# Performance work log

Measured on AMD Instinct MI355X. Metric: run time of the kernel, lower is better.

Reference implementation:

```python
import jax, jax.numpy as jnp
import numpy as np

BIG = 1e30  # stands in for sys.maxsize in fp32-safe form


def _find_neg_anchors(e_actv, host):
    # Full pairwise Euclidean distance matrix (equivalent to the
    # pdist -> triangular reconstruction in the torch code).
    sq = jnp.sum(e_actv * e_actv, axis=1)                       # [n]
    d2 = sq[:, None] + sq[None, :] - 2.0 * (e_actv @ e_actv.T)  # [n, n]
    dist = jnp.sqrt(jnp.maximum(d2, 0.0))
    n = e_actv.shape[0]
    # mask: self (diagonal) and same-discriminator pairs -> huge distance
    same_discr = host[:, None] == host[None, :]
    eye = jnp.eye(n, dtype=bool)
    dist = jnp.where(same_discr | eye, BIG, dist)
    idxs = jnp.argmin(dist, axis=1)                             # [n]
    return e_actv[idxs]                                         # gather


def setup_inputs() -> dict:
    key = jax.random.key(0)
    k1, k2, k3 = jax.random.split(key, 3)
    n, d = 8192, 256
    e_actv = jax.random.normal(k1, (n, d), dtype=jnp.float32)
    e_ap = jax.random.normal(k2, (n, d), dtype=jnp.float32)
    host = jax.random.randint(k3, (n,), 0, 64, dtype=jnp.int64 if jax.config.read('jax_enable_x64') else jnp.int32)
    return {"e_actv": e_actv, "e_ap": e_ap, "host": host}


def reference(e_actv, e_ap, host):
    # forward returns (e_actv, e_ap, e_an); e_an computed under no_grad
    e_an = jax.lax.stop_gradient(_find_neg_anchors(e_actv, host))
    return (e_actv, e_ap, e_an)
```

## Files before the change

### kernel.cpp

```cpp
#include <hip/hip_runtime.h>
#include <hip/hip_bf16.h>
#include <cmath>
#include <cstddef>

#define N 8192
#define D 256
#define BIR 128
#define BJC 64
#define NBLK 4160

typedef __attribute__((ext_vector_type(8))) short short8;
typedef __attribute__((ext_vector_type(4))) float float4v;

__device__ inline ushort f2bf(float x) {
    __hip_bfloat16 h = __float2bfloat16(x);
    return __builtin_bit_cast(ushort, h);
}
__device__ inline float bf2f(ushort u) {
    __hip_bfloat16 h = __builtin_bit_cast(__hip_bfloat16, u);
    return __bfloat162float(h);
}

__device__ inline unsigned long long packKI(float k, int idx) {
    unsigned u = __float_as_uint(k);
    u = (u & 0x80000000u) ? ~u : (u | 0x80000000u);
    return ((unsigned long long)u << 32) | (unsigned)idx;
}


__global__ void prep_kernel(const float4* __restrict__ a, const float4* __restrict__ p,
                            float4* __restrict__ out, float* __restrict__ sq,
                            ushort* __restrict__ Ehi, ushort* __restrict__ Elo,
                            unsigned long long* __restrict__ M) {
    const int gsz = gridDim.x * blockDim.x;
    const int g0 = blockIdx.x * blockDim.x + threadIdx.x;
    const int total = N * D / 4;

    for (int idx = g0; idx < total; idx += gsz) {
        float4 v = a[idx];
        out[idx] = v;
        float s = v.x * v.x + v.y * v.y + v.z * v.z + v.w * v.w;
        #pragma unroll
        for (int off = 32; off; off >>= 1) s += __shfl_down(s, off);
        if ((threadIdx.x & 63) == 0) sq[idx >> 6] = s;
    }
    for (int idx = g0; idx < total; idx += gsz) out[total + idx] = p[idx];

    {
        const int w = g0 >> 6;
        if (w < 4096) {
            const int lane = threadIdx.x & 63;
            const int tx = lane & 15;
            const int q  = lane >> 4;
            const int r16 = w >> 3;
            const int ktc = w & 7;
            const int row = r16 * 16 + tx;
            const float4 v0 = a[row * 64 + ktc * 8 + q * 2];
            const float4 v1 = a[row * 64 + ktc * 8 + q * 2 + 1];
            float e[8] = {v0.x, v0.y, v0.z, v0.w, v1.x, v1.y, v1.z, v1.w};
            short8 hs, ls;
            #pragma unroll
            for (int j = 0; j < 8; j++) {
                ushort h = f2bf(e[j]);
                ushort l = f2bf(e[j] - bf2f(h));
                hs[j] = (short)h;
                ls[j] = (short)l;
            }
            const size_t off = (size_t)(r16 * 8 + ktc) * 512 + lane * 8;
            *(short8*)&Ehi[off] = hs;
            *(short8*)&Elo[off] = ls;
        }
    }
    for (int i = g0; i < N; i += gsz) M[i] = 0xFFFFFFFFFFFFFFFFull;
}

__launch_bounds__(256, 4)
__global__ void argmin_sym(const ushort* __restrict__ Ehi, const ushort* __restrict__ Elo,
                           const int* __restrict__ host, const float* __restrict__ sq,
                           unsigned long long* __restrict__ M) {
    const int b0 = blockIdx.x;
    const int b = (b0 & 7) * (NBLK / 8) + (b0 >> 3);

    int g, p;
    if (b < 1808)      { g = 0; p = b; }
    else if (b < 3104) { g = 1; p = b - 1808; }
    else if (b < 3888) { g = 2; p = b - 3104; }
    else               { g = 3; p = b - 3888; }
    int d, i;
    if (p >= 240) {
        d = 30 + ((p - 240) >> 4);
        i = (p - 240) & 15;
    } else {
        int m = (int)sqrtf((float)p);
        while (m * m > p) m--;
        while ((m + 1) * (m + 1) <= p) m++;
        if (p >= m * m + m) { d = 2 * m;     i = p - (m * m + m); }
        else                { d = 2 * m - 1; i = p - m * m; }
    }
    const int ti = 16 * g + i;
    const int tj = 32 * g + d;

    __shared__ float sqA_s[BIR];
    __shared__ float sqB_s[BJC];
    __shared__ int   hostB_s[BJC];
    __shared__ float rowV[2 * BIR]; __shared__ int rowI[2 * BIR];
    __shared__ float colV[2 * BJC]; __shared__ int colI[2 * BJC];

    const int ib0 = ti * BIR;
    const int jb0 = tj * BJC;
    const int tid = threadIdx.x;
    const int lane = tid & 63;
    const int wave = tid >> 6;
    const int wrow = wave >> 1;
    const int wcol = wave & 1;
    const int tx = lane & 15;
    const int q  = lane >> 4;

    if (tid < BIR) sqA_s[tid] = sq[ib0 + tid];
    if (tid < BJC) {
        sqB_s[tid] = sq[jb0 + tid];
        hostB_s[tid] = host[jb0 + tid];
    }

    unsigned hostAp[4];
    #pragma unroll
    for (int rt = 0; rt < 4; rt++) {
        unsigned pk = 0;
        #pragma unroll
        for (int reg = 0; reg < 4; reg++) {
            int hv = host[ib0 + wrow * 64 + rt * 16 + q * 4 + reg];
            pk |= ((unsigned)hv & 0xFFu) << (8 * reg);
        }
        hostAp[rt] = pk;
    }

    float4v acc[4][2];
    #pragma unroll
    for (int rt = 0; rt < 4; rt++)
        #pragma unroll
        for (int ct = 0; ct < 2; ct++) acc[rt][ct] = (float4v)(0.0f);

    const int pA = (ib0 >> 4) + wrow * 4;
    const int pB = (jb0 >> 4) + wcol * 2;
    const int lo8 = lane * 8;

    int obA[4], obB[2];
    #pragma unroll
    for (int rt = 0; rt < 4; rt++) obA[rt] = (((pA + rt) * 8) * 512 + lo8) * 2;
    #pragma unroll
    for (int ct = 0; ct < 2; ct++) obB[ct] = (((pB + ct) * 8) * 512 + lo8) * 2;
    const char* EhiB = (const char*)Ehi;
    const char* EloB = (const char*)Elo;

    short8 aH[4], aL[4], bH[2], bL[2];

    #pragma unroll
    for (int k = 0; k < 8; k++) {
        #pragma unroll
        for (int rt = 0; rt < 4; rt++) {
            aH[rt] = *(const short8*)(EhiB + obA[rt]);
            aL[rt] = *(const short8*)(EloB + obA[rt]);
        }
        #pragma unroll
        for (int ct = 0; ct < 2; ct++) {
            bH[ct] = *(const short8*)(EhiB + obB[ct]);
            bL[ct] = *(const short8*)(EloB + obB[ct]);
        }
        #pragma unroll
        for (int rt = 0; rt < 4; rt++) obA[rt] += 1024;
        #pragma unroll
        for (int ct = 0; ct < 2; ct++) obB[ct] += 1024;
        __builtin_amdgcn_sched_barrier(0);
        #pragma unroll
        for (int rt = 0; rt < 4; rt++)
            #pragma unroll
            for (int ct = 0; ct < 2; ct++)
                acc[rt][ct] = __builtin_amdgcn_mfma_f32_16x16x32_bf16(aH[rt], bH[ct], acc[rt][ct], 0, 0, 0);
        #pragma unroll
        for (int rt = 0; rt < 4; rt++)
            #pragma unroll
            for (int ct = 0; ct < 2; ct++)
                acc[rt][ct] = __builtin_amdgcn_mfma_f32_16x16x32_bf16(aH[rt], bL[ct], acc[rt][ct], 0, 0, 0);
        #pragma unroll
        for (int rt = 0; rt < 4; rt++)
            #pragma unroll
            for (int ct = 0; ct < 2; ct++)
                acc[rt][ct] = __builtin_amdgcn_mfma_f32_16x16x32_bf16(aL[rt], bH[ct], acc[rt][ct], 0, 0, 0);
        __builtin_amdgcn_sched_barrier(0);
    }

    __syncthreads();

    #pragma unroll
    for (int rt = 0; rt < 4; rt++) {
        unsigned hp = hostAp[rt];
        #pragma unroll
        for (int reg = 0; reg < 4; reg++) {
            int il = wrow * 64 + rt * 16 + q * 4 + reg;
            int ig = ib0 + il;
            int ha = (int)((hp >> (8 * reg)) & 0xFFu);
            float v = 3.0e38f; int ix = 0x7fffffff;
            #pragma unroll
            for (int ct = 0; ct < 2; ct++) {
                int jl = wcol * 32 + ct * 16 + tx;
                int jg = jb0 + jl;
                float key = sqB_s[jl] - 2.0f * acc[rt][ct][reg];
                bool masked = (hostB_s[jl] == ha) || (jg <= ig);
                if (!masked && (key < v || (key == v && jg < ix))) { v = key; ix = jg; }
            }
            #pragma unroll
            for (int dd = 1; dd < 16; dd <<= 1) {
                float ov = __shfl_xor(v, dd);
                int   oi = __shfl_xor(ix, dd);
                if (ov < v || (ov == v && oi < ix)) { v = ov; ix = oi; }
            }
            if (tx == 0) { rowV[il * 2 + wcol] = v; rowI[il * 2 + wcol] = ix; }
        }
    }

    #pragma unroll
    for (int ct = 0; ct < 2; ct++) {
        int jl = wcol * 32 + ct * 16 + tx;
        int jg = jb0 + jl;
        int hb = hostB_s[jl];
        float v = 3.0e38f; int ix = 0x7fffffff;
        #pragma unroll
        for (int rt = 0; rt < 4; rt++) {
            unsigned hp = hostAp[rt];
            #pragma unroll
            for (int reg = 0; reg < 4; reg++) {
                int il = wrow * 64 + rt * 16 + q * 4 + reg;
                int ig = ib0 + il;
                bool masked = ((int)((hp >> (8 * reg)) & 0xFFu) == hb) || (ig >= jg);
                float key = sqA_s[il] - 2.0f * acc[rt][ct][reg];
                if (!masked && (key < v || (key == v && ig < ix))) { v = key; ix = ig; }
            }
        }
        #pragma unroll
        for (int dd = 16; dd < 64; dd <<= 1) {
            float ov = __shfl_xor(v, dd);
            int   oi = __shfl_xor(ix, dd);
            if (ov < v || (ov == v && oi < ix)) { v = ov; ix = oi; }
        }
        if (q == 0) { colV[jl * 2 + wrow] = v; colI[jl * 2 + wrow] = ix; }
    }

    __syncthreads();
    if (tid < BIR) {
        float v0 = rowV[tid * 2];     int x0 = rowI[tid * 2];
        float v1 = rowV[tid * 2 + 1]; int x1 = rowI[tid * 2 + 1];
        if (v1 < v0 || (v1 == v0 && x1 < x0)) { v0 = v1; x0 = x1; }
        atomicMin(&M[ib0 + tid], packKI(v0, x0));
    }
    if (tid < BJC) {
        float w0 = colV[tid * 2];     int y0 = colI[tid * 2];
        float w1 = colV[tid * 2 + 1]; int y1 = colI[tid * 2 + 1];
        if (w1 < w0 || (w1 == w0 && y1 < y0)) { w0 = w1; y0 = y1; }
        atomicMin(&M[jb0 + tid], packKI(w0, y0));
    }
}

__global__ void finalize_kernel(const unsigned long long* __restrict__ M,
                                const float* __restrict__ E, float* __restrict__ out_an) {
    int row = blockIdx.x;
    int t = threadIdx.x;
    int idx = (int)(unsigned)(M[row] & 0xFFFFFFFFull);
    float4 v = *(const float4*)&E[(size_t)idx * D + t * 4];
    *(float4*)&out_an[(size_t)row * D + t * 4] = v;
}

extern "C" void kernel_launch(void* const* d_in, const int* in_sizes, int n_in,
                              void* d_out, int out_size, void* d_ws, size_t ws_size,
                              hipStream_t stream) {
    const float* e_actv = (const float*)d_in[0];
    const float* e_ap   = (const float*)d_in[1];
    const int*   host   = (const int*)d_in[2];
    float* out = (float*)d_out;

    unsigned long long* M = (unsigned long long*)d_ws;
    float*  sq  = (float*)(M + N);
    ushort* Ehi = (ushort*)(sq + N);
    ushort* Elo = Ehi + (size_t)N * D;

    prep_kernel<<<1024, 256, 0, stream>>>(
        (const float4*)e_actv, (const float4*)e_ap, (float4*)out,
        sq, Ehi, Elo, M);
    argmin_sym<<<NBLK, 256, 0, stream>>>(Ehi, Elo, host, sq, M);
    finalize_kernel<<<N, 64, 0, stream>>>(M, e_actv, out + 2 * (size_t)N * D);
}
```

Measured before the change: 166.4 us.

## Use square 128x128 upper-triangle tiles with two column halves per block

Changes the symmetric tile decomposition from 128x64 tiles (4160 blocks) to 128x128 square tiles over the upper triangle (2080 blocks). Each block processes its column range in two 64-wide halves, reusing the row panel and keeping per-row running minima in registers as packed 64-bit keys. This halves the number of blocks and the per-block setup and atomic cost, and improves reuse of A fragments. In exchange it raises register pressure (launch bounds drop from 4 to 3 waves per SIMD) and serializes two accumulation passes within a block.

```diff
diff --git a/kernel.cpp b/kernel.cpp
--- a/kernel.cpp
+++ b/kernel.cpp
@@ -6,11 +6,12 @@
 #define N 8192
 #define D 256
 #define BIR 128
-#define BJC 64
-#define NBLK 4160
+#define NPAIR 2080
 
 typedef __attribute__((ext_vector_type(8))) short short8;
 typedef __attribute__((ext_vector_type(4))) float float4v;
+
+#define U64MAX 0xFFFFFFFFFFFFFFFFull
 
 __device__ inline ushort f2bf(float x) {
     __hip_bfloat16 h = __float2bfloat16(x);
@@ -25,6 +26,9 @@
     unsigned u = __float_as_uint(k);
     u = (u & 0x80000000u) ? ~u : (u | 0x80000000u);
     return ((unsigned long long)u << 32) | (unsigned)idx;
+}
+__device__ inline unsigned long long min64(unsigned long long a, unsigned long long b) {
+    return a < b ? a : b;
 }
 
 
@@ -74,40 +78,39 @@
     for (int i = g0; i < N; i += gsz) M[i] = 0xFFFFFFFFFFFFFFFFull;
 }
 
-__launch_bounds__(256, 4)
+__launch_bounds__(256, 3)
 __global__ void argmin_sym(const ushort* __restrict__ Ehi, const ushort* __restrict__ Elo,
                            const int* __restrict__ host, const float* __restrict__ sq,
                            unsigned long long* __restrict__ M) {
     const int b0 = blockIdx.x;
-    const int b = (b0 & 7) * (NBLK / 8) + (b0 >> 3);
+    const int b = (b0 & 7) * (NPAIR / 8) + (b0 >> 3);
 
     int g, p;
-    if (b < 1808)      { g = 0; p = b; }
-    else if (b < 3104) { g = 1; p = b - 1808; }
-    else if (b < 3888) { g = 2; p = b - 3104; }
-    else               { g = 3; p = b - 3888; }
-    int d, i;
-    if (p >= 240) {
-        d = 30 + ((p - 240) >> 4);
-        i = (p - 240) & 15;
+    if (b < 904)       { g = 0; p = b; }
+    else if (b < 1552) { g = 1; p = b - 904; }
+    else if (b < 1944) { g = 2; p = b - 1552; }
+    else               { g = 3; p = b - 1944; }
+    int dd, i;
+    if (p >= 136) {
+        dd = 16 + ((p - 136) >> 4);
+        i = (p - 136) & 15;
     } else {
-        int m = (int)sqrtf((float)p);
-        while (m * m > p) m--;
-        while ((m + 1) * (m + 1) <= p) m++;
-        if (p >= m * m + m) { d = 2 * m;     i = p - (m * m + m); }
-        else                { d = 2 * m - 1; i = p - m * m; }
-    }
-    const int ti = 16 * g + i;
-    const int tj = 32 * g + d;
+        int m = (int)((sqrtf(8.0f * (float)p + 1.0f) - 1.0f) * 0.5f);
+        while ((m + 1) * (m + 2) / 2 <= p) m++;
+        while (m * (m + 1) / 2 > p) m--;
+        dd = m; i = p - m * (m + 1) / 2;
+    }
+    const int ti  = 16 * g + i;
+    const int tjj = 16 * g + dd;
 
     __shared__ float sqA_s[BIR];
-    __shared__ float sqB_s[BJC];
-    __shared__ int   hostB_s[BJC];
-    __shared__ float rowV[2 * BIR]; __shared__ int rowI[2 * BIR];
-    __shared__ float colV[2 * BJC]; __shared__ int colI[2 * BJC];
+    __shared__ float sqB_s[BIR];
+    __shared__ int   hostB_s[BIR];
+    __shared__ unsigned long long rowU[2 * BIR];
+    __shared__ unsigned long long colU[2 * BIR];
 
     const int ib0 = ti * BIR;
-    const int jb0 = tj * BJC;
+    const int jb0 = tjj * BIR;
     const int tid = threadIdx.x;
     const int lane = tid & 63;
     const int wave = tid >> 6;
@@ -116,8 +119,8 @@
     const int tx = lane & 15;
     const int q  = lane >> 4;
 
-    if (tid < BIR) sqA_s[tid] = sq[ib0 + tid];
-    if (tid < BJC) {
+    if (tid < BIR) {
+        sqA_s[tid] = sq[ib0 + tid];
         sqB_s[tid] = sq[jb0 + tid];
         hostB_s[tid] = host[jb0 + tid];
     }
@@ -133,130 +136,132 @@
         }
         hostAp[rt] = pk;
     }
-
-    float4v acc[4][2];
-    #pragma unroll
-    for (int rt = 0; rt < 4; rt++)
-        #pragma unroll
-        for (int ct = 0; ct < 2; ct++) acc[rt][ct] = (float4v)(0.0f);
+    __syncthreads();
 
     const int pA = (ib0 >> 4) + wrow * 4;
-    const int pB = (jb0 >> 4) + wcol * 2;
-    const int lo8 = lane * 8;
-
-    int obA[4], obB[2];
-    #pragma unroll
-    for (int rt = 0; rt < 4; rt++) obA[rt] = (((pA + rt) * 8) * 512 + lo8) * 2;
-    #pragma unroll
-    for (int ct = 0; ct < 2; ct++) obB[ct] = (((pB + ct) * 8) * 512 + lo8) * 2;
+    const int lo8b = lane * 16;
     const char* EhiB = (const char*)Ehi;
     const char* EloB = (const char*)Elo;
 
+    unsigned long long rmin[16];
+    #pragma unroll
+    for (int t = 0; t < 16; t++) rmin[t] = U64MAX;
+
+    float4v acc[4][2];
     short8 aH[4], aL[4], bH[2], bL[2];
 
     #pragma unroll
-    for (int k = 0; k < 8; k++) {
-        #pragma unroll
-        for (int rt = 0; rt < 4; rt++) {
-            aH[rt] = *(const short8*)(EhiB + obA[rt]);
-            aL[rt] = *(const short8*)(EloB + obA[rt]);
-        }
-        #pragma unroll
-        for (int ct = 0; ct < 2; ct++) {
-            bH[ct] = *(const short8*)(EhiB + obB[ct]);
-            bL[ct] = *(const short8*)(EloB + obB[ct]);
-        }
-        #pragma unroll
-        for (int rt = 0; rt < 4; rt++) obA[rt] += 1024;
-        #pragma unroll
-        for (int ct = 0; ct < 2; ct++) obB[ct] += 1024;
-        __builtin_amdgcn_sched_barrier(0);
+    for (int h = 0; h < 2; h++) {
+        int obA[4], obB[2];
+        #pragma unroll
+        for (int rt = 0; rt < 4; rt++) obA[rt] = ((pA + rt) * 8) * 1024 + lo8b;
+        #pragma unroll
+        for (int ct = 0; ct < 2; ct++) obB[ct] = ((tjj * 8 + h * 4 + wcol * 2 + ct) * 8) * 1024 + lo8b;
         #pragma unroll
         for (int rt = 0; rt < 4; rt++)
             #pragma unroll
-            for (int ct = 0; ct < 2; ct++)
-                acc[rt][ct] = __builtin_amdgcn_mfma_f32_16x16x32_bf16(aH[rt], bH[ct], acc[rt][ct], 0, 0, 0);
-        #pragma unroll
-        for (int rt = 0; rt < 4; rt++)
-            #pragma unroll
-            for (int ct = 0; ct < 2; ct++)
-                acc[rt][ct] = __builtin_amdgcn_mfma_f32_16x16x32_bf16(aH[rt], bL[ct], acc[rt][ct], 0, 0, 0);
-        #pragma unroll
-        for (int rt = 0; rt < 4; rt++)
-            #pragma unroll
-            for (int ct = 0; ct < 2; ct++)
-                acc[rt][ct] = __builtin_amdgcn_mfma_f32_16x16x32_bf16(aL[rt], bH[ct], acc[rt][ct], 0, 0, 0);
-        __builtin_amdgcn_sched_barrier(0);
-    }
-
-    __syncthreads();
-
-    #pragma unroll
-    for (int rt = 0; rt < 4; rt++) {
-        unsigned hp = hostAp[rt];
-        #pragma unroll
-        for (int reg = 0; reg < 4; reg++) {
-            int il = wrow * 64 + rt * 16 + q * 4 + reg;
-            int ig = ib0 + il;
-            int ha = (int)((hp >> (8 * reg)) & 0xFFu);
-            float v = 3.0e38f; int ix = 0x7fffffff;
+            for (int ct = 0; ct < 2; ct++) acc[rt][ct] = (float4v)(0.0f);
+
+        #pragma unroll
+        for (int k = 0; k < 8; k++) {
+            #pragma unroll
+            for (int rt = 0; rt < 4; rt++) {
+                aH[rt] = *(const short8*)(EhiB + obA[rt]);
+                aL[rt] = *(const short8*)(EloB + obA[rt]);
+            }
             #pragma unroll
             for (int ct = 0; ct < 2; ct++) {
-                int jl = wcol * 32 + ct * 16 + tx;
-                int jg = jb0 + jl;
-                float key = sqB_s[jl] - 2.0f * acc[rt][ct][reg];
-                bool masked = (hostB_s[jl] == ha) || (jg <= ig);
-                if (!masked && (key < v || (key == v && jg < ix))) { v = key; ix = jg; }
-            }
-            #pragma unroll
-            for (int dd = 1; dd < 16; dd <<= 1) {
-                float ov = __shfl_xor(v, dd);
-                int   oi = __shfl_xor(ix, dd);
-                if (ov < v || (ov == v && oi < ix)) { v = ov; ix = oi; }
-            }
-            if (tx == 0) { rowV[il * 2 + wcol] = v; rowI[il * 2 + wcol] = ix; }
-        }
-    }
-
-    #pragma unroll
-    for (int ct = 0; ct < 2; ct++) {
-        int jl = wcol * 32 + ct * 16 + tx;
-        int jg = jb0 + jl;
-        int hb = hostB_s[jl];
-        float v = 3.0e38f; int ix = 0x7fffffff;
+                bH[ct] = *(const short8*)(EhiB + obB[ct]);
+                bL[ct] = *(const short8*)(EloB + obB[ct]);
+            }
+            #pragma unroll
+            for (int rt = 0; rt < 4; rt++) obA[rt] += 1024;
+            #pragma unroll
+            for (int ct = 0; ct < 2; ct++) obB[ct] += 1024;
+            __builtin_amdgcn_sched_barrier(0);
+            #pragma unroll
+            for (int rt = 0; rt < 4; rt++)
+                #pragma unroll
+                for (int ct = 0; ct < 2; ct++)
+                    acc[rt][ct] = __builtin_amdgcn_mfma_f32_16x16x32_bf16(aH[rt], bH[ct], acc[rt][ct], 0, 0, 0);
+            #pragma unroll
+            for (int rt = 0; rt < 4; rt++)
+                #pragma unroll
+                for (int ct = 0; ct < 2; ct++)
+                    acc[rt][ct] = __builtin_amdgcn_mfma_f32_16x16x32_bf16(aH[rt], bL[ct], acc[rt][ct], 0, 0, 0);
+            #pragma unroll
+            for (int rt = 0; rt < 4; rt++)
+                #pragma unroll
+                for (int ct = 0; ct < 2; ct++)
+                    acc[rt][ct] = __builtin_amdgcn_mfma_f32_16x16x32_bf16(aL[rt], bH[ct], acc[rt][ct], 0, 0, 0);
+            __builtin_amdgcn_sched_barrier(0);
+        }
+
         #pragma unroll
         for (int rt = 0; rt < 4; rt++) {
             unsigned hp = hostAp[rt];
             #pragma unroll
             for (int reg = 0; reg < 4; reg++) {
-                int il = wrow * 64 + rt * 16 + q * 4 + reg;
-                int ig = ib0 + il;
-                bool masked = ((int)((hp >> (8 * reg)) & 0xFFu) == hb) || (ig >= jg);
-                float key = sqA_s[il] - 2.0f * acc[rt][ct][reg];
-                if (!masked && (key < v || (key == v && ig < ix))) { v = key; ix = ig; }
-            }
-        }
-        #pragma unroll
-        for (int dd = 16; dd < 64; dd <<= 1) {
-            float ov = __shfl_xor(v, dd);
-            int   oi = __shfl_xor(ix, dd);
-            if (ov < v || (ov == v && oi < ix)) { v = ov; ix = oi; }
-        }
-        if (q == 0) { colV[jl * 2 + wrow] = v; colI[jl * 2 + wrow] = ix; }
+                const int il = wrow * 64 + rt * 16 + q * 4 + reg;
+                const int ig = ib0 + il;
+                const int ha = (int)((hp >> (8 * reg)) & 0xFFu);
+                #pragma unroll
+                for (int ct = 0; ct < 2; ct++) {
+                    const int jl = h * 64 + wcol * 32 + ct * 16 + tx;
+                    const int jg = jb0 + jl;
+                    const float key = sqB_s[jl] - 2.0f * acc[rt][ct][reg];
+                    const bool masked = (hostB_s[jl] == ha) || (jg <= ig);
+                    if (!masked) rmin[rt * 4 + reg] = min64(rmin[rt * 4 + reg], packKI(key, jg));
+                }
+            }
+        }
+        #pragma unroll
+        for (int ct = 0; ct < 2; ct++) {
+            const int jl = h * 64 + wcol * 32 + ct * 16 + tx;
+            const int jg = jb0 + jl;
+            const int hb = hostB_s[jl];
+            float v = 3.0e38f; int ix = 0x7fffffff;
+            #pragma unroll
+            for (int rt = 0; rt < 4; rt++) {
+                unsigned hp = hostAp[rt];
+                #pragma unroll
+                for (int reg = 0; reg < 4; reg++) {
+                    const int il = wrow * 64 + rt * 16 + q * 4 + reg;
+                    const int ig = ib0 + il;
+                    const bool masked = ((int)((hp >> (8 * reg)) & 0xFFu) == hb) || (ig >= jg);
+                    const float key = sqA_s[il] - 2.0f * acc[rt][ct][reg];
+                    if (!masked && (key < v || (key == v && ig < ix))) { v = key; ix = ig; }
+                }
+            }
+            #pragma unroll
+            for (int s = 16; s < 64; s <<= 1) {
+                float ov = __shfl_xor(v, s);
+                int   oi = __shfl_xor(ix, s);
+                if (ov < v || (ov == v && oi < ix)) { v = ov; ix = oi; }
+            }
+            if (q == 0) colU[jl * 2 + wrow] = packKI(v, ix);
+        }
+    }
+
+    #pragma unroll
+    for (int rt = 0; rt < 4; rt++) {
+        #pragma unroll
+        for (int reg = 0; reg < 4; reg++) {
+            unsigned long long m = rmin[rt * 4 + reg];
+            #pragma unroll
+            for (int s = 1; s < 16; s <<= 1)
+                m = min64(m, (unsigned long long)__shfl_xor((unsigned long long)m, s));
+            if (tx == 0) {
+                const int il = wrow * 64 + rt * 16 + q * 4 + reg;
+                rowU[il * 2 + wcol] = m;
+            }
+        }
     }
 
     __syncthreads();
     if (tid < BIR) {
-        float v0 = rowV[tid * 2];     int x0 = rowI[tid * 2];
-        float v1 = rowV[tid * 2 + 1]; int x1 = rowI[tid * 2 + 1];
-        if (v1 < v0 || (v1 == v0 && x1 < x0)) { v0 = v1; x0 = x1; }
-        atomicMin(&M[ib0 + tid], packKI(v0, x0));
-    }
-    if (tid < BJC) {
-        float w0 = colV[tid * 2];     int y0 = colI[tid * 2];
-        float w1 = colV[tid * 2 + 1]; int y1 = colI[tid * 2 + 1];
-        if (w1 < w0 || (w1 == w0 && y1 < y0)) { w0 = w1; y0 = y1; }
-        atomicMin(&M[jb0 + tid], packKI(w0, y0));
+        atomicMin(&M[ib0 + tid], min64(rowU[tid * 2], rowU[tid * 2 + 1]));
+        atomicMin(&M[jb0 + tid], min64(colU[tid * 2], colU[tid * 2 + 1]));
     }
 }
 
@@ -285,6 +290,6 @@
     prep_kernel<<<1024, 256, 0, stream>>>(
         (const float4*)e_actv, (const float4*)e_ap, (float4*)out,
         sq, Ehi, Elo, M);
-    argmin_sym<<<NBLK, 256, 0, stream>>>(Ehi, Elo, host, sq, M);
+    argmin_sym<<<NPAIR, 256, 0, stream>>>(Ehi, Elo, host, sq, M);
     finalize_kernel<<<N, 64, 0, stream>>>(M, e_actv, out + 2 * (size_t)N * D);
 }
```

After: 370.1 us. 122% more time.
